# Performance work log

Hardware: AMD Instinct MI355X
Metric: run time of the kernel (lower is better)

The kernel has to match this reference:

```python
import jax, jax.numpy as jnp
import numpy as np

HIDDEN = 256
IN = 72  # 9*8
NUM_STEPS = 8


def setup_inputs() -> dict:
    key = jax.random.key(0)
    ks = jax.random.split(key, 12)
    s = 1.0 / np.sqrt(HIDDEN)
    B = 32768
    return {
        "z": jax.random.normal(ks[0], (1, B, HIDDEN), dtype=jnp.float32),
        # LSTM (torch layout): gates order i, f, g, o
        "W_ih": jax.random.uniform(ks[1], (4 * HIDDEN, IN), minval=-s, maxval=s),
        "W_hh": jax.random.uniform(ks[2], (4 * HIDDEN, HIDDEN), minval=-s, maxval=s),
        "b_ih": jax.random.uniform(ks[3], (4 * HIDDEN,), minval=-s, maxval=s),
        "b_hh": jax.random.uniform(ks[4], (4 * HIDDEN,), minval=-s, maxval=s),
        # Linear h: 256 -> 256
        "Wh": jax.random.uniform(ks[5], (HIDDEN, HIDDEN), minval=-s, maxval=s),
        "bh": jax.random.uniform(ks[6], (HIDDEN,), minval=-s, maxval=s),
        # Linear c: 256 -> 256
        "Wc": jax.random.uniform(ks[7], (HIDDEN, HIDDEN), minval=-s, maxval=s),
        "bc": jax.random.uniform(ks[8], (HIDDEN,), minval=-s, maxval=s),
        # Linear hout: 256 -> 72
        "Wo": jax.random.uniform(ks[9], (IN, HIDDEN), minval=-s, maxval=s),
        "bo": jax.random.uniform(ks[10], (IN,), minval=-s, maxval=s),
    }


def reference(z, W_ih, W_hh, b_ih, b_hh, Wh, bh, Wc, bc, Wo, bo):
    B = z.shape[1]
    z0 = z[0]                           # (B, 256)
    h = z0 @ Wh.T + bh                  # initial hidden state
    c = z0 @ Wc.T + bc                  # initial cell state
    x = jnp.zeros((B, IN), dtype=z.dtype)

    def step(carry, _):
        x, h, c = carry
        gates = x @ W_ih.T + b_ih + h @ W_hh.T + b_hh   # (B, 1024)
        i, f, g, o = jnp.split(gates, 4, axis=-1)
        i = jax.nn.sigmoid(i)
        f = jax.nn.sigmoid(f)
        g = jnp.tanh(g)
        o = jax.nn.sigmoid(o)
        c = f * c + i * g
        h = o * jnp.tanh(c)
        y = jax.nn.sigmoid(h @ Wo.T + bo)               # (B, 72), fed back as next input
        return (y, h, c), y

    _, ys = jax.lax.scan(step, (x, h, c), None, length=NUM_STEPS)  # (8, B, 72)
    return jnp.transpose(ys, (1, 0, 2))                             # (B, 8, 72)
```

## Files before the change

### kernel.cpp

```cpp
#include <hip/hip_runtime.h>
#include <hip/hip_bf16.h>

#define HID   256
#define NGATE 1024
#define INP   72
#define INPP  96
#define STEPS 8
#define TB    64
#define LDH   264
#define LDX   104

#define OFF_WHH 0
#define OFF_WIH 262144
#define OFF_WH  360448
#define OFF_WC  425984
#define OFF_WO  491520
#define N_BF    512000
#define OFF_BG_BYTES 1024000
#define OFF_STAGE_BYTES (1u << 20)

typedef short  s8_t  __attribute__((ext_vector_type(8)));
typedef float  f4_t  __attribute__((ext_vector_type(4)));

static __device__ __forceinline__ unsigned short f2bf(float f) {
  unsigned int u = __float_as_uint(f);
  u = (u + 0x7FFFu + ((u >> 16) & 1u)) >> 16;
  return (unsigned short)u;
}
static __device__ __forceinline__ float fast_rcp(float x) {
#if __has_builtin(__builtin_amdgcn_rcpf)
  return __builtin_amdgcn_rcpf(x);
#else
  return 1.f / x;
#endif
}
static __device__ __forceinline__ float sigm(float x) {
  return fast_rcp(1.f + __expf(-x));
}
static __device__ __forceinline__ float tanh_(float x) {
  float t = fminf(-2.f * x, 88.f);
  float e = __expf(t);
  return (1.f - e) * fast_rcp(1.f + e);
}

__global__ void prep_kernel(const float* __restrict__ Wih, const float* __restrict__ Whh,
                            const float* __restrict__ bih, const float* __restrict__ bhh,
                            const float* __restrict__ Wh, const float* __restrict__ Wc,
                            const float* __restrict__ Wo,
                            unsigned short* __restrict__ wsh, float* __restrict__ bg) {
  int stride = gridDim.x * blockDim.x;
  for (int i = blockIdx.x * blockDim.x + threadIdx.x; i < N_BF + NGATE; i += stride) {
    if (i < OFF_WIH) {
      wsh[i] = f2bf(Whh[i]);
    } else if (i < OFF_WH) {
      int j = i - OFF_WIH; int n = j / INPP; int k = j - n * INPP;
      wsh[i] = (k < INP) ? f2bf(Wih[n * INP + k]) : (unsigned short)0;
    } else if (i < OFF_WC) {
      wsh[i] = f2bf(Wh[i - OFF_WH]);
    } else if (i < OFF_WO) {
      wsh[i] = f2bf(Wc[i - OFF_WC]);
    } else if (i < N_BF) {
      int j = i - OFF_WO; int t = j >> 8; int k = j & 255;
      wsh[i] = (t < INP) ? f2bf(Wo[t * HID + k]) : (unsigned short)0;
    } else {
      int j = i - N_BF;
      bg[j] = bih[j] + bhh[j];
    }
  }
}

template <int STAGED>
__global__ __launch_bounds__(512, 2) void lstm_kernel(
    const float* __restrict__ z, const unsigned short* __restrict__ wsh,
    const float* __restrict__ bg, const float* __restrict__ bh,
    const float* __restrict__ bc, const float* __restrict__ bo,
    float* __restrict__ out, float* __restrict__ stage, int NB) {
  __shared__ unsigned short h_lds[TB * LDH];
  __shared__ unsigned short x_lds[TB * LDX];

  const int tid  = threadIdx.x;
  const int w    = tid >> 6;
  const int lane = tid & 63;
  const int lq   = lane >> 4;
  const int ln   = lane & 15;
  const int rb   = blockIdx.x * TB;
  const int colh0 = w * 32 + ln;

  const unsigned short* whh_l = wsh + OFF_WHH + colh0 * HID  + lq * 8;
  const unsigned short* wih_l = wsh + OFF_WIH + colh0 * INPP + lq * 8;
  const unsigned short* wh_l  = wsh + OFF_WH  + colh0 * HID  + lq * 8;
  const unsigned short* wc_l  = wsh + OFF_WC  + colh0 * HID  + lq * 8;
  const unsigned short* h_rd  = &h_lds[ln * LDH + lq * 8];
  const unsigned short* x_rd  = &x_lds[ln * LDX + lq * 8];
  unsigned short*       h_wr  = &h_lds[(lq * 4) * LDH + colh0];

  for (int i = tid; i < TB * LDX; i += 512) x_lds[i] = 0;

  f4_t acc_h[4][2], acc_c[4][2];
  #pragma unroll
  for (int rt = 0; rt < 4; ++rt)
    #pragma unroll
    for (int ct = 0; ct < 2; ++ct) {
      acc_h[rt][ct] = {0.f, 0.f, 0.f, 0.f};
      acc_c[rt][ct] = {0.f, 0.f, 0.f, 0.f};
    }

  const float* z_l = z + (size_t)(rb + ln) * HID + lq * 8;

  #pragma unroll 2
  for (int kc = 0; kc < 8; ++kc) {
    s8_t a[4];
    #pragma unroll
    for (int rt = 0; rt < 4; ++rt) {
      f4_t v0 = *reinterpret_cast<const f4_t*>(z_l + rt * 16 * HID + kc * 32);
      f4_t v1 = *reinterpret_cast<const f4_t*>(z_l + rt * 16 * HID + kc * 32 + 4);
      s8_t av;
      av[0] = (short)f2bf(v0[0]); av[1] = (short)f2bf(v0[1]);
      av[2] = (short)f2bf(v0[2]); av[3] = (short)f2bf(v0[3]);
      av[4] = (short)f2bf(v1[0]); av[5] = (short)f2bf(v1[1]);
      av[6] = (short)f2bf(v1[2]); av[7] = (short)f2bf(v1[3]);
      a[rt] = av;
    }
    #pragma unroll
    for (int ct = 0; ct < 2; ++ct) {
      s8_t bhf = *reinterpret_cast<const s8_t*>(wh_l + ct * 16 * HID + kc * 32);
      s8_t bcf = *reinterpret_cast<const s8_t*>(wc_l + ct * 16 * HID + kc * 32);
      #pragma unroll
      for (int rt = 0; rt < 4; ++rt) {
        acc_h[rt][ct] = __builtin_amdgcn_mfma_f32_16x16x32_bf16(a[rt], bhf, acc_h[rt][ct], 0, 0, 0);
        acc_c[rt][ct] = __builtin_amdgcn_mfma_f32_16x16x32_bf16(a[rt], bcf, acc_c[rt][ct], 0, 0, 0);
      }
    }
  }

  float c_reg[4][2][4];
  #pragma unroll
  for (int ct = 0; ct < 2; ++ct) {
    const float bhv = bh[colh0 + ct * 16];
    const float bcv = bc[colh0 + ct * 16];
    #pragma unroll
    for (int rt = 0; rt < 4; ++rt)
      #pragma unroll
      for (int r = 0; r < 4; ++r) {
        float hv = acc_h[rt][ct][r] + bhv;
        c_reg[rt][ct][r] = acc_c[rt][ct][r] + bcv;
        h_wr[(rt * 16 + r) * LDH + ct * 16] = f2bf(hv);
      }
  }
  __syncthreads();

  float biasg[4][2];
  #pragma unroll
  for (int q = 0; q < 4; ++q)
    #pragma unroll
    for (int ct = 0; ct < 2; ++ct)
      biasg[q][ct] = bg[q * 256 + colh0 + ct * 16];

  const int colY = w * 16 + ln;
  float bov = 0.f;
  const unsigned short* wo_l = wsh + OFF_WO + lq * 8;
  if (w < 5) {
    wo_l += colY * HID;
    if (colY < INP) bov = bo[colY];
  }

  for (int s = 0; s < STEPS; ++s) {
    f4_t acc[4][4][2];
    #pragma unroll
    for (int q = 0; q < 4; ++q)
      #pragma unroll
      for (int rt = 0; rt < 4; ++rt)
        #pragma unroll
        for (int ct = 0; ct < 2; ++ct) {
          const float b = biasg[q][ct];
          acc[q][rt][ct] = {b, b, b, b};
        }

    #pragma unroll 2
    for (int kc = 0; kc < 8; ++kc) {
      s8_t a[4];
      #pragma unroll
      for (int rt = 0; rt < 4; ++rt)
        a[rt] = *reinterpret_cast<const s8_t*>(h_rd + rt * 16 * LDH + kc * 32);
      #pragma unroll
      for (int q = 0; q < 4; ++q)
        #pragma unroll
        for (int ct = 0; ct < 2; ++ct) {
          s8_t bfr = *reinterpret_cast<const s8_t*>(whh_l + (q * 256 + ct * 16) * HID + kc * 32);
          #pragma unroll
          for (int rt = 0; rt < 4; ++rt)
            acc[q][rt][ct] = __builtin_amdgcn_mfma_f32_16x16x32_bf16(a[rt], bfr, acc[q][rt][ct], 0, 0, 0);
        }
    }
    #pragma unroll
    for (int kc = 0; kc < 3; ++kc) {
      s8_t a[4];
      #pragma unroll
      for (int rt = 0; rt < 4; ++rt)
        a[rt] = *reinterpret_cast<const s8_t*>(x_rd + rt * 16 * LDX + kc * 32);
      #pragma unroll
      for (int q = 0; q < 4; ++q)
        #pragma unroll
        for (int ct = 0; ct < 2; ++ct) {
          s8_t bfr = *reinterpret_cast<const s8_t*>(wih_l + (q * 256 + ct * 16) * INPP + kc * 32);
          #pragma unroll
          for (int rt = 0; rt < 4; ++rt)
            acc[q][rt][ct] = __builtin_amdgcn_mfma_f32_16x16x32_bf16(a[rt], bfr, acc[q][rt][ct], 0, 0, 0);
        }
    }
    __syncthreads();

    #pragma unroll
    for (int rt = 0; rt < 4; ++rt)
      #pragma unroll
      for (int ct = 0; ct < 2; ++ct)
        #pragma unroll
        for (int r = 0; r < 4; ++r) {
          float iv = sigm(acc[0][rt][ct][r]);
          float fv = sigm(acc[1][rt][ct][r]);
          float gv = tanh_(acc[2][rt][ct][r]);
          float ov = sigm(acc[3][rt][ct][r]);
          float cn = fv * c_reg[rt][ct][r] + iv * gv;
          c_reg[rt][ct][r] = cn;
          float hv = ov * tanh_(cn);
          h_wr[(rt * 16 + r) * LDH + ct * 16] = f2bf(hv);
        }
    __syncthreads();

    if (w < 5) {
      f4_t accy[4];
      #pragma unroll
      for (int rt = 0; rt < 4; ++rt) accy[rt] = {bov, bov, bov, bov};
      #pragma unroll 2
      for (int kc = 0; kc < 8; ++kc) {
        s8_t bfr = *reinterpret_cast<const s8_t*>(wo_l + kc * 32);
        #pragma unroll
        for (int rt = 0; rt < 4; ++rt) {
          s8_t a = *reinterpret_cast<const s8_t*>(h_rd + rt * 16 * LDH + kc * 32);
          accy[rt] = __builtin_amdgcn_mfma_f32_16x16x32_bf16(a, bfr, accy[rt], 0, 0, 0);
        }
      }
      if (colY < INP) {
        float* st_base;
        if (STAGED) {
          st_base = stage + (((size_t)s * NB + blockIdx.x) * TB + lq * 4) * INP + colY;
        } else {
          st_base = out + (size_t)(rb + lq * 4) * (STEPS * INP) + s * INP + colY;
        }
        unsigned short* x_wr = &x_lds[(lq * 4) * LDX + colY];
        #pragma unroll
        for (int rt = 0; rt < 4; ++rt)
          #pragma unroll
          for (int r = 0; r < 4; ++r) {
            float yv = sigm(accy[rt][r]);
            if (STAGED) {
              st_base[(size_t)(rt * 16 + r) * INP] = yv;
            } else {
              st_base[(size_t)(rt * 16 + r) * (STEPS * INP)] = yv;
            }
            x_wr[(rt * 16 + r) * LDX] = f2bf(yv);
          }
      }
    }
    __syncthreads();
  }
}

__global__ __launch_bounds__(512) void reorder_kernel(
    const float* __restrict__ stage, float* __restrict__ out, int NB) {
  const int lane = threadIdx.x & 63;
  const int row  = blockIdx.x * 8 + (threadIdx.x >> 6);
  const int b    = row >> 6;
  const int r    = row & 63;
  #pragma unroll
  for (int i = lane; i < STEPS * INP; i += 64) {
    int s = i / INP;
    int c = i - s * INP;
    out[(size_t)row * (STEPS * INP) + i] =
        stage[(((size_t)s * NB + b) * TB + r) * INP + c];
  }
}

extern "C" void kernel_launch(void* const* d_in, const int* in_sizes, int n_in,
                              void* d_out, int out_size, void* d_ws, size_t ws_size,
                              hipStream_t stream) {
  const float* z   = (const float*)d_in[0];
  const float* Wih = (const float*)d_in[1];
  const float* Whh = (const float*)d_in[2];
  const float* bih = (const float*)d_in[3];
  const float* bhh = (const float*)d_in[4];
  const float* Wh  = (const float*)d_in[5];
  const float* bh  = (const float*)d_in[6];
  const float* Wc  = (const float*)d_in[7];
  const float* bc  = (const float*)d_in[8];
  const float* Wo  = (const float*)d_in[9];
  const float* bo  = (const float*)d_in[10];
  float* out = (float*)d_out;

  unsigned short* wsh = (unsigned short*)d_ws;
  float* bg    = (float*)((char*)d_ws + OFF_BG_BYTES);
  float* stage = (float*)((char*)d_ws + OFF_STAGE_BYTES);

  const int B  = in_sizes[0] / HID;
  const int NB = B / TB;

  hipLaunchKernelGGL(prep_kernel, dim3(512), dim3(256), 0, stream,
                     Wih, Whh, bih, bhh, Wh, Wc, Wo, wsh, bg);

  const size_t stage_need = (size_t)OFF_STAGE_BYTES + (size_t)B * STEPS * INP * 4;
  if (ws_size >= stage_need) {
    hipLaunchKernelGGL((lstm_kernel<1>), dim3(NB), dim3(512), 0, stream,
                       z, wsh, bg, bh, bc, bo, out, stage, NB);
    hipLaunchKernelGGL(reorder_kernel, dim3(B / 8), dim3(512), 0, stream,
                       stage, out, NB);
  } else {
    hipLaunchKernelGGL((lstm_kernel<0>), dim3(NB), dim3(512), 0, stream,
                       z, wsh, bg, bh, bc, bo, out, stage, NB);
  }
}
```

Before: 680.7 us.

## Shrink LSTM row tile to 32 rows with 4 waves of 64 columns each

The batch tile per block drops from 64 to 32 rows and the block from 8 waves to 4, so each wave now owns 64 hidden columns over 2 row tiles instead of 32 columns over 4 row tiles. The output projection is remapped so all 4 waves compute 16 output columns each, and wave 0 computes the remaining 8. The aim is twice as many blocks, for better load balance across CUs and smaller LDS per block. In exchange each block streams the full recurrent weight matrix for half as many rows, doubling weight traffic per row, and wave 0 carries extra projection work that lengthens the serial step.

```diff
diff --git a/kernel.cpp b/kernel.cpp
--- a/kernel.cpp
+++ b/kernel.cpp
@@ -6,7 +6,8 @@
 #define INP   72
 #define INPP  96
 #define STEPS 8
-#define TB    64
+#define TB    32
+#define NTHR  256
 #define LDH   264
 #define LDX   104
 
@@ -70,7 +71,7 @@
 }
 
 template <int STAGED>
-__global__ __launch_bounds__(512, 2) void lstm_kernel(
+__global__ __launch_bounds__(NTHR, 2) void lstm_kernel(
     const float* __restrict__ z, const unsigned short* __restrict__ wsh,
     const float* __restrict__ bg, const float* __restrict__ bh,
     const float* __restrict__ bc, const float* __restrict__ bo,
@@ -84,7 +85,7 @@
   const int lq   = lane >> 4;
   const int ln   = lane & 15;
   const int rb   = blockIdx.x * TB;
-  const int colh0 = w * 32 + ln;
+  const int colh0 = w * 64 + ln;
 
   const unsigned short* whh_l = wsh + OFF_WHH + colh0 * HID  + lq * 8;
   const unsigned short* wih_l = wsh + OFF_WIH + colh0 * INPP + lq * 8;
@@ -94,13 +95,13 @@
   const unsigned short* x_rd  = &x_lds[ln * LDX + lq * 8];
   unsigned short*       h_wr  = &h_lds[(lq * 4) * LDH + colh0];
 
-  for (int i = tid; i < TB * LDX; i += 512) x_lds[i] = 0;
-
-  f4_t acc_h[4][2], acc_c[4][2];
+  for (int i = tid; i < TB * LDX; i += NTHR) x_lds[i] = 0;
+
+  f4_t acc_h[2][4], acc_c[2][4];
   #pragma unroll
-  for (int rt = 0; rt < 4; ++rt)
-    #pragma unroll
-    for (int ct = 0; ct < 2; ++ct) {
+  for (int rt = 0; rt < 2; ++rt)
+    #pragma unroll
+    for (int ct = 0; ct < 4; ++ct) {
       acc_h[rt][ct] = {0.f, 0.f, 0.f, 0.f};
       acc_c[rt][ct] = {0.f, 0.f, 0.f, 0.f};
     }
@@ -109,9 +110,9 @@
 
   #pragma unroll 2
   for (int kc = 0; kc < 8; ++kc) {
-    s8_t a[4];
-    #pragma unroll
-    for (int rt = 0; rt < 4; ++rt) {
+    s8_t a[2];
+    #pragma unroll
+    for (int rt = 0; rt < 2; ++rt) {
       f4_t v0 = *reinterpret_cast<const f4_t*>(z_l + rt * 16 * HID + kc * 32);
       f4_t v1 = *reinterpret_cast<const f4_t*>(z_l + rt * 16 * HID + kc * 32 + 4);
       s8_t av;
@@ -122,24 +123,24 @@
       a[rt] = av;
     }
     #pragma unroll
-    for (int ct = 0; ct < 2; ++ct) {
+    for (int ct = 0; ct < 4; ++ct) {
       s8_t bhf = *reinterpret_cast<const s8_t*>(wh_l + ct * 16 * HID + kc * 32);
       s8_t bcf = *reinterpret_cast<const s8_t*>(wc_l + ct * 16 * HID + kc * 32);
       #pragma unroll
-      for (int rt = 0; rt < 4; ++rt) {
+      for (int rt = 0; rt < 2; ++rt) {
         acc_h[rt][ct] = __builtin_amdgcn_mfma_f32_16x16x32_bf16(a[rt], bhf, acc_h[rt][ct], 0, 0, 0);
         acc_c[rt][ct] = __builtin_amdgcn_mfma_f32_16x16x32_bf16(a[rt], bcf, acc_c[rt][ct], 0, 0, 0);
       }
     }
   }
 
-  float c_reg[4][2][4];
+  float c_reg[2][4][4];
   #pragma unroll
-  for (int ct = 0; ct < 2; ++ct) {
+  for (int ct = 0; ct < 4; ++ct) {
     const float bhv = bh[colh0 + ct * 16];
     const float bcv = bc[colh0 + ct * 16];
     #pragma unroll
-    for (int rt = 0; rt < 4; ++rt)
+    for (int rt = 0; rt < 2; ++rt)
       #pragma unroll
       for (int r = 0; r < 4; ++r) {
         float hv = acc_h[rt][ct][r] + bhv;
@@ -149,71 +150,70 @@
   }
   __syncthreads();
 
-  float biasg[4][2];
+  float biasg[4][4];
   #pragma unroll
   for (int q = 0; q < 4; ++q)
     #pragma unroll
-    for (int ct = 0; ct < 2; ++ct)
+    for (int ct = 0; ct < 4; ++ct)
       biasg[q][ct] = bg[q * 256 + colh0 + ct * 16];
 
   const int colY = w * 16 + ln;
-  float bov = 0.f;
-  const unsigned short* wo_l = wsh + OFF_WO + lq * 8;
-  if (w < 5) {
-    wo_l += colY * HID;
-    if (colY < INP) bov = bo[colY];
-  }
+  const float bov = bo[colY];
+  const unsigned short* wo_l  = wsh + OFF_WO + colY * HID + lq * 8;
+  const int colY2 = 64 + ln;
+  const float bov2 = (colY2 < INP) ? bo[colY2] : 0.f;
+  const unsigned short* wo2_l = wsh + OFF_WO + colY2 * HID + lq * 8;
 
   for (int s = 0; s < STEPS; ++s) {
-    f4_t acc[4][4][2];
+    f4_t acc[4][2][4];
     #pragma unroll
     for (int q = 0; q < 4; ++q)
       #pragma unroll
-      for (int rt = 0; rt < 4; ++rt)
-        #pragma unroll
-        for (int ct = 0; ct < 2; ++ct) {
+      for (int rt = 0; rt < 2; ++rt)
+        #pragma unroll
+        for (int ct = 0; ct < 4; ++ct) {
           const float b = biasg[q][ct];
           acc[q][rt][ct] = {b, b, b, b};
         }
 
     #pragma unroll 2
     for (int kc = 0; kc < 8; ++kc) {
-      s8_t a[4];
-      #pragma unroll
-      for (int rt = 0; rt < 4; ++rt)
+      s8_t a[2];
+      #pragma unroll
+      for (int rt = 0; rt < 2; ++rt)
         a[rt] = *reinterpret_cast<const s8_t*>(h_rd + rt * 16 * LDH + kc * 32);
       #pragma unroll
       for (int q = 0; q < 4; ++q)
         #pragma unroll
-        for (int ct = 0; ct < 2; ++ct) {
+        for (int ct = 0; ct < 4; ++ct) {
           s8_t bfr = *reinterpret_cast<const s8_t*>(whh_l + (q * 256 + ct * 16) * HID + kc * 32);
           #pragma unroll
-          for (int rt = 0; rt < 4; ++rt)
+          for (int rt = 0; rt < 2; ++rt)
             acc[q][rt][ct] = __builtin_amdgcn_mfma_f32_16x16x32_bf16(a[rt], bfr, acc[q][rt][ct], 0, 0, 0);
         }
     }
     #pragma unroll
     for (int kc = 0; kc < 3; ++kc) {
-      s8_t a[4];
-      #pragma unroll
-      for (int rt = 0; rt < 4; ++rt)
+      s8_t a[2];
+      #pragma unroll
+      for (int rt = 0; rt < 2; ++rt)
         a[rt] = *reinterpret_cast<const s8_t*>(x_rd + rt * 16 * LDX + kc * 32);
       #pragma unroll
       for (int q = 0; q < 4; ++q)
         #pragma unroll
-        for (int ct = 0; ct < 2; ++ct) {
+        for (int ct = 0; ct < 4; ++ct) {
           s8_t bfr = *reinterpret_cast<const s8_t*>(wih_l + (q * 256 + ct * 16) * INPP + kc * 32);
           #pragma unroll
-          for (int rt = 0; rt < 4; ++rt)
+          for (int rt = 0; rt < 2; ++rt)
             acc[q][rt][ct] = __builtin_amdgcn_mfma_f32_16x16x32_bf16(a[rt], bfr, acc[q][rt][ct], 0, 0, 0);
         }
     }
     __syncthreads();
 
     #pragma unroll
-    for (int rt = 0; rt < 4; ++rt)
-      #pragma unroll
-      for (int ct = 0; ct < 2; ++ct)
+    for (int rt = 0; rt < 2; ++rt)
+      #pragma unroll
+      for (int ct = 0; ct < 4; ++ct)
         #pragma unroll
         for (int r = 0; r < 4; ++r) {
           float iv = sigm(acc[0][rt][ct][r]);
@@ -227,29 +227,62 @@
         }
     __syncthreads();
 
-    if (w < 5) {
-      f4_t accy[4];
-      #pragma unroll
-      for (int rt = 0; rt < 4; ++rt) accy[rt] = {bov, bov, bov, bov};
+    {
+      f4_t accy[2];
+      #pragma unroll
+      for (int rt = 0; rt < 2; ++rt) accy[rt] = {bov, bov, bov, bov};
       #pragma unroll 2
       for (int kc = 0; kc < 8; ++kc) {
         s8_t bfr = *reinterpret_cast<const s8_t*>(wo_l + kc * 32);
         #pragma unroll
-        for (int rt = 0; rt < 4; ++rt) {
+        for (int rt = 0; rt < 2; ++rt) {
           s8_t a = *reinterpret_cast<const s8_t*>(h_rd + rt * 16 * LDH + kc * 32);
           accy[rt] = __builtin_amdgcn_mfma_f32_16x16x32_bf16(a, bfr, accy[rt], 0, 0, 0);
         }
       }
-      if (colY < INP) {
+      float* st_base;
+      if (STAGED) {
+        st_base = stage + (((size_t)s * NB + blockIdx.x) * TB + lq * 4) * INP + colY;
+      } else {
+        st_base = out + (size_t)(rb + lq * 4) * (STEPS * INP) + s * INP + colY;
+      }
+      unsigned short* x_wr = &x_lds[(lq * 4) * LDX + colY];
+      #pragma unroll
+      for (int rt = 0; rt < 2; ++rt)
+        #pragma unroll
+        for (int r = 0; r < 4; ++r) {
+          float yv = sigm(accy[rt][r]);
+          if (STAGED) {
+            st_base[(size_t)(rt * 16 + r) * INP] = yv;
+          } else {
+            st_base[(size_t)(rt * 16 + r) * (STEPS * INP)] = yv;
+          }
+          x_wr[(rt * 16 + r) * LDX] = f2bf(yv);
+        }
+    }
+    if (w == 0) {
+      f4_t accy[2];
+      #pragma unroll
+      for (int rt = 0; rt < 2; ++rt) accy[rt] = {bov2, bov2, bov2, bov2};
+      #pragma unroll 2
+      for (int kc = 0; kc < 8; ++kc) {
+        s8_t bfr = *reinterpret_cast<const s8_t*>(wo2_l + kc * 32);
+        #pragma unroll
+        for (int rt = 0; rt < 2; ++rt) {
+          s8_t a = *reinterpret_cast<const s8_t*>(h_rd + rt * 16 * LDH + kc * 32);
+          accy[rt] = __builtin_amdgcn_mfma_f32_16x16x32_bf16(a, bfr, accy[rt], 0, 0, 0);
+        }
+      }
+      if (colY2 < INP) {
         float* st_base;
         if (STAGED) {
-          st_base = stage + (((size_t)s * NB + blockIdx.x) * TB + lq * 4) * INP + colY;
+          st_base = stage + (((size_t)s * NB + blockIdx.x) * TB + lq * 4) * INP + colY2;
         } else {
-          st_base = out + (size_t)(rb + lq * 4) * (STEPS * INP) + s * INP + colY;
-        }
-        unsigned short* x_wr = &x_lds[(lq * 4) * LDX + colY];
-        #pragma unroll
-        for (int rt = 0; rt < 4; ++rt)
+          st_base = out + (size_t)(rb + lq * 4) * (STEPS * INP) + s * INP + colY2;
+        }
+        unsigned short* x_wr = &x_lds[(lq * 4) * LDX + colY2];
+        #pragma unroll
+        for (int rt = 0; rt < 2; ++rt)
           #pragma unroll
           for (int r = 0; r < 4; ++r) {
             float yv = sigm(accy[rt][r]);
@@ -270,8 +303,8 @@
     const float* __restrict__ stage, float* __restrict__ out, int NB) {
   const int lane = threadIdx.x & 63;
   const int row  = blockIdx.x * 8 + (threadIdx.x >> 6);
-  const int b    = row >> 6;
-  const int r    = row & 63;
+  const int b    = row >> 5;
+  const int r    = row & 31;
   #pragma unroll
   for (int i = lane; i < STEPS * INP; i += 64) {
     int s = i / INP;
@@ -309,12 +342,12 @@
 
   const size_t stage_need = (size_t)OFF_STAGE_BYTES + (size_t)B * STEPS * INP * 4;
   if (ws_size >= stage_need) {
-    hipLaunchKernelGGL((lstm_kernel<1>), dim3(NB), dim3(512), 0, stream,
+    hipLaunchKernelGGL((lstm_kernel<1>), dim3(NB), dim3(NTHR), 0, stream,
                        z, wsh, bg, bh, bc, bo, out, stage, NB);
     hipLaunchKernelGGL(reorder_kernel, dim3(B / 8), dim3(512), 0, stream,
                        stage, out, NB);
   } else {
-    hipLaunchKernelGGL((lstm_kernel<0>), dim3(NB), dim3(512), 0, stream,
+    hipLaunchKernelGGL((lstm_kernel<0>), dim3(NB), dim3(NTHR), 0, stream,
                        z, wsh, bg, bh, bc, bo, out, stage, NB);
   }
 }
```

After: 1.092 ms. +60.4%, slower.

## Double block to 1024 threads and pre-swizzle weights into per-lane MFMA fragment order

Applied to the files above, without the earlier changes.

The block grows from 8 to 16 waves, and each wave now owns 16 hidden columns instead of 32. This halves the per-thread accumulator count, which lowers register pressure and allows more waves per CU (launch bounds 1024,4). The prep kernel rewrites all bf16 weights into a per-wave, per-lane fragment order so each B-fragment load is one fully contiguous 16-byte-per-lane read. The cost is more waves contending at each __syncthreads, and all 16 waves still stream the full weight set from L2 every step.

```diff
diff --git a/kernel.cpp b/kernel.cpp
--- a/kernel.cpp
+++ b/kernel.cpp
@@ -4,20 +4,18 @@
 #define HID   256
 #define NGATE 1024
 #define INP   72
-#define INPP  96
 #define STEPS 8
 #define TB    64
+#define NTHR  1024
 #define LDH   264
 #define LDX   104
 
-#define OFF_WHH 0
-#define OFF_WIH 262144
-#define OFF_WH  360448
-#define OFF_WC  425984
-#define OFF_WO  491520
-#define N_BF    512000
-#define OFF_BG_BYTES 1024000
-#define OFF_STAGE_BYTES (1u << 20)
+#define WSEQ2 32768
+#define OFF_WHI 524288
+#define OFF_WCI 589824
+#define N_ALL   655360
+#define OFF_BG_BYTES    1310720
+#define OFF_STAGE_BYTES 1314816
 
 typedef short  s8_t  __attribute__((ext_vector_type(8)));
 typedef float  f4_t  __attribute__((ext_vector_type(4)));
@@ -49,28 +47,58 @@
                             const float* __restrict__ Wo,
                             unsigned short* __restrict__ wsh, float* __restrict__ bg) {
   int stride = gridDim.x * blockDim.x;
-  for (int i = blockIdx.x * blockDim.x + threadIdx.x; i < N_BF + NGATE; i += stride) {
-    if (i < OFF_WIH) {
-      wsh[i] = f2bf(Whh[i]);
-    } else if (i < OFF_WH) {
-      int j = i - OFF_WIH; int n = j / INPP; int k = j - n * INPP;
-      wsh[i] = (k < INP) ? f2bf(Wih[n * INP + k]) : (unsigned short)0;
-    } else if (i < OFF_WC) {
-      wsh[i] = f2bf(Wh[i - OFF_WH]);
-    } else if (i < OFF_WO) {
-      wsh[i] = f2bf(Wc[i - OFF_WC]);
-    } else if (i < N_BF) {
-      int j = i - OFF_WO; int t = j >> 8; int k = j & 255;
-      wsh[i] = (t < INP) ? f2bf(Wo[t * HID + k]) : (unsigned short)0;
+  for (int i = blockIdx.x * blockDim.x + threadIdx.x; i < N_ALL + NGATE; i += stride) {
+    if (i < N_ALL) {
+      float v = 0.f;
+      if (i < OFF_WHI) {
+        int w  = i >> 15;
+        int r  = i & 32767;
+        int f  = r >> 9;
+        int e  = r & 511;
+        int lane = e >> 3, j = e & 7;
+        int lq = lane >> 4, ln = lane & 15;
+        int kk = lq * 8 + j;
+        if (f < 32) {
+          int kc = f >> 2, q = f & 3;
+          int g  = q * 256 + w * 16 + ln;
+          int k  = kc * 32 + kk;
+          v = Whh[g * HID + k];
+        } else if (f < 44) {
+          int t  = f - 32;
+          int kc = t >> 2, q = t & 3;
+          int g  = q * 256 + w * 16 + ln;
+          int k  = kc * 32 + kk;
+          v = (k < INP) ? Wih[g * INP + k] : 0.f;
+        } else if (f < 52) {
+          int kc = f - 44;
+          int c  = w * 16 + ln;
+          int k  = kc * 32 + kk;
+          v = (w < 5 && c < INP) ? Wo[c * HID + k] : 0.f;
+        }
+      } else {
+        int base = (i < OFF_WCI) ? OFF_WHI : OFF_WCI;
+        const float* Wsrc = (i < OFF_WCI) ? Wh : Wc;
+        int jj = i - base;
+        int w  = jj >> 12;
+        int r  = jj & 4095;
+        int kc = r >> 9;
+        int e  = r & 511;
+        int lane = e >> 3, j = e & 7;
+        int lq = lane >> 4, ln = lane & 15;
+        int c  = w * 16 + ln;
+        int k  = kc * 32 + lq * 8 + j;
+        v = Wsrc[c * HID + k];
+      }
+      wsh[i] = f2bf(v);
     } else {
-      int j = i - N_BF;
-      bg[j] = bih[j] + bhh[j];
+      int jb = i - N_ALL;
+      bg[jb] = bih[jb] + bhh[jb];
     }
   }
 }
 
 template <int STAGED>
-__global__ __launch_bounds__(512, 2) void lstm_kernel(
+__global__ __launch_bounds__(NTHR, 4) void lstm_kernel(
     const float* __restrict__ z, const unsigned short* __restrict__ wsh,
     const float* __restrict__ bg, const float* __restrict__ bh,
     const float* __restrict__ bc, const float* __restrict__ bo,
@@ -84,26 +112,23 @@
   const int lq   = lane >> 4;
   const int ln   = lane & 15;
   const int rb   = blockIdx.x * TB;
-  const int colh0 = w * 32 + ln;
-
-  const unsigned short* whh_l = wsh + OFF_WHH + colh0 * HID  + lq * 8;
-  const unsigned short* wih_l = wsh + OFF_WIH + colh0 * INPP + lq * 8;
-  const unsigned short* wh_l  = wsh + OFF_WH  + colh0 * HID  + lq * 8;
-  const unsigned short* wc_l  = wsh + OFF_WC  + colh0 * HID  + lq * 8;
-  const unsigned short* h_rd  = &h_lds[ln * LDH + lq * 8];
-  const unsigned short* x_rd  = &x_lds[ln * LDX + lq * 8];
-  unsigned short*       h_wr  = &h_lds[(lq * 4) * LDH + colh0];
-
-  for (int i = tid; i < TB * LDX; i += 512) x_lds[i] = 0;
-
-  f4_t acc_h[4][2], acc_c[4][2];
+  const int colh0 = w * 16 + ln;
+
+  const unsigned short* wst = wsh + w * WSEQ2 + lane * 8;
+  const unsigned short* whi = wsh + OFF_WHI + w * 4096 + lane * 8;
+  const unsigned short* wci = wsh + OFF_WCI + w * 4096 + lane * 8;
+  const unsigned short* h_rd = &h_lds[ln * LDH + lq * 8];
+  const unsigned short* x_rd = &x_lds[ln * LDX + lq * 8];
+  unsigned short*       h_wr = &h_lds[(lq * 4) * LDH + colh0];
+
+  for (int i = tid; i < TB * LDX; i += NTHR) x_lds[i] = 0;
+
+  f4_t acc_h[4], acc_c[4];
   #pragma unroll
-  for (int rt = 0; rt < 4; ++rt)
-    #pragma unroll
-    for (int ct = 0; ct < 2; ++ct) {
-      acc_h[rt][ct] = {0.f, 0.f, 0.f, 0.f};
-      acc_c[rt][ct] = {0.f, 0.f, 0.f, 0.f};
-    }
+  for (int rt = 0; rt < 4; ++rt) {
+    acc_h[rt] = {0.f, 0.f, 0.f, 0.f};
+    acc_c[rt] = {0.f, 0.f, 0.f, 0.f};
+  }
 
   const float* z_l = z + (size_t)(rb + ln) * HID + lq * 8;
 
@@ -121,60 +146,47 @@
       av[6] = (short)f2bf(v1[2]); av[7] = (short)f2bf(v1[3]);
       a[rt] = av;
     }
-    #pragma unroll
-    for (int ct = 0; ct < 2; ++ct) {
-      s8_t bhf = *reinterpret_cast<const s8_t*>(wh_l + ct * 16 * HID + kc * 32);
-      s8_t bcf = *reinterpret_cast<const s8_t*>(wc_l + ct * 16 * HID + kc * 32);
-      #pragma unroll
-      for (int rt = 0; rt < 4; ++rt) {
-        acc_h[rt][ct] = __builtin_amdgcn_mfma_f32_16x16x32_bf16(a[rt], bhf, acc_h[rt][ct], 0, 0, 0);
-        acc_c[rt][ct] = __builtin_amdgcn_mfma_f32_16x16x32_bf16(a[rt], bcf, acc_c[rt][ct], 0, 0, 0);
-      }
-    }
-  }
-
-  float c_reg[4][2][4];
-  #pragma unroll
-  for (int ct = 0; ct < 2; ++ct) {
-    const float bhv = bh[colh0 + ct * 16];
-    const float bcv = bc[colh0 + ct * 16];
+    s8_t bhf = *reinterpret_cast<const s8_t*>(whi + kc * 512);
+    s8_t bcf = *reinterpret_cast<const s8_t*>(wci + kc * 512);
+    #pragma unroll
+    for (int rt = 0; rt < 4; ++rt) {
+      acc_h[rt] = __builtin_amdgcn_mfma_f32_16x16x32_bf16(a[rt], bhf, acc_h[rt], 0, 0, 0);
+      acc_c[rt] = __builtin_amdgcn_mfma_f32_16x16x32_bf16(a[rt], bcf, acc_c[rt], 0, 0, 0);
+    }
+  }
+
+  float c_reg[4][4];
+  {
+    const float bhv = bh[colh0];
+    const float bcv = bc[colh0];
     #pragma unroll
     for (int rt = 0; rt < 4; ++rt)
       #pragma unroll
       for (int r = 0; r < 4; ++r) {
-        float hv = acc_h[rt][ct][r] + bhv;
-        c_reg[rt][ct][r] = acc_c[rt][ct][r] + bcv;
-        h_wr[(rt * 16 + r) * LDH + ct * 16] = f2bf(hv);
+        float hv = acc_h[rt][r] + bhv;
+        c_reg[rt][r] = acc_c[rt][r] + bcv;
+        h_wr[(rt * 16 + r) * LDH] = f2bf(hv);
       }
   }
   __syncthreads();
 
-  float biasg[4][2];
+  float biasg[4];
   #pragma unroll
   for (int q = 0; q < 4; ++q)
-    #pragma unroll
-    for (int ct = 0; ct < 2; ++ct)
-      biasg[q][ct] = bg[q * 256 + colh0 + ct * 16];
-
-  const int colY = w * 16 + ln;
+    biasg[q] = bg[q * 256 + colh0];
+
   float bov = 0.f;
-  const unsigned short* wo_l = wsh + OFF_WO + lq * 8;
-  if (w < 5) {
-    wo_l += colY * HID;
-    if (colY < INP) bov = bo[colY];
-  }
+  if (w < 5 && colh0 < INP) bov = bo[colh0];
 
   for (int s = 0; s < STEPS; ++s) {
-    f4_t acc[4][4][2];
+    f4_t acc[4][4];
     #pragma unroll
     for (int q = 0; q < 4; ++q)
       #pragma unroll
-      for (int rt = 0; rt < 4; ++rt)
-        #pragma unroll
-        for (int ct = 0; ct < 2; ++ct) {
-          const float b = biasg[q][ct];
-          acc[q][rt][ct] = {b, b, b, b};
-        }
+      for (int rt = 0; rt < 4; ++rt) {
+        const float b = biasg[q];
+        acc[q][rt] = {b, b, b, b};
+      }
 
     #pragma unroll 2
     for (int kc = 0; kc < 8; ++kc) {
@@ -183,14 +195,12 @@
       for (int rt = 0; rt < 4; ++rt)
         a[rt] = *reinterpret_cast<const s8_t*>(h_rd + rt * 16 * LDH + kc * 32);
       #pragma unroll
-      for (int q = 0; q < 4; ++q)
+      for (int q = 0; q < 4; ++q) {
+        s8_t bfr = *reinterpret_cast<const s8_t*>(wst + (kc * 4 + q) * 512);
         #pragma unroll
-        for (int ct = 0; ct < 2; ++ct) {
-          s8_t bfr = *reinterpret_cast<const s8_t*>(whh_l + (q * 256 + ct * 16) * HID + kc * 32);
-          #pragma unroll
-          for (int rt = 0; rt < 4; ++rt)
-            acc[q][rt][ct] = __builtin_amdgcn_mfma_f32_16x16x32_bf16(a[rt], bfr, acc[q][rt][ct], 0, 0, 0);
-        }
+        for (int rt = 0; rt < 4; ++rt)
+          acc[q][rt] = __builtin_amdgcn_mfma_f32_16x16x32_bf16(a[rt], bfr, acc[q][rt], 0, 0, 0);
+      }
     }
     #pragma unroll
     for (int kc = 0; kc < 3; ++kc) {
@@ -199,32 +209,28 @@
       for (int rt = 0; rt < 4; ++rt)
         a[rt] = *reinterpret_cast<const s8_t*>(x_rd + rt * 16 * LDX + kc * 32);
       #pragma unroll
-      for (int q = 0; q < 4; ++q)
+      for (int q = 0; q < 4; ++q) {
+        s8_t bfr = *reinterpret_cast<const s8_t*>(wst + (32 + kc * 4 + q) * 512);
         #pragma unroll
-        for (int ct = 0; ct < 2; ++ct) {
-          s8_t bfr = *reinterpret_cast<const s8_t*>(wih_l + (q * 256 + ct * 16) * INPP + kc * 32);
-          #pragma unroll
-          for (int rt = 0; rt < 4; ++rt)
-            acc[q][rt][ct] = __builtin_amdgcn_mfma_f32_16x16x32_bf16(a[rt], bfr, acc[q][rt][ct], 0, 0, 0);
-        }
+        for (int rt = 0; rt < 4; ++rt)
+          acc[q][rt] = __builtin_amdgcn_mfma_f32_16x16x32_bf16(a[rt], bfr, acc[q][rt], 0, 0, 0);
+      }
     }
     __syncthreads();
 
     #pragma unroll
     for (int rt = 0; rt < 4; ++rt)
       #pragma unroll
-      for (int ct = 0; ct < 2; ++ct)
-        #pragma unroll
-        for (int r = 0; r < 4; ++r) {
-          float iv = sigm(acc[0][rt][ct][r]);
-          float fv = sigm(acc[1][rt][ct][r]);
-          float gv = tanh_(acc[2][rt][ct][r]);
-          float ov = sigm(acc[3][rt][ct][r]);
-          float cn = fv * c_reg[rt][ct][r] + iv * gv;
-          c_reg[rt][ct][r] = cn;
-          float hv = ov * tanh_(cn);
-          h_wr[(rt * 16 + r) * LDH + ct * 16] = f2bf(hv);
-        }
+      for (int r = 0; r < 4; ++r) {
+        float iv = sigm(acc[0][rt][r]);
+        float fv = sigm(acc[1][rt][r]);
+        float gv = tanh_(acc[2][rt][r]);
+        float ov = sigm(acc[3][rt][r]);
+        float cn = fv * c_reg[rt][r] + iv * gv;
+        c_reg[rt][r] = cn;
+        float hv = ov * tanh_(cn);
+        h_wr[(rt * 16 + r) * LDH] = f2bf(hv);
+      }
     __syncthreads();
 
     if (w < 5) {
@@ -233,21 +239,21 @@
       for (int rt = 0; rt < 4; ++rt) accy[rt] = {bov, bov, bov, bov};
       #pragma unroll 2
       for (int kc = 0; kc < 8; ++kc) {
-        s8_t bfr = *reinterpret_cast<const s8_t*>(wo_l + kc * 32);
+        s8_t bfr = *reinterpret_cast<const s8_t*>(wst + (44 + kc) * 512);
         #pragma unroll
         for (int rt = 0; rt < 4; ++rt) {
           s8_t a = *reinterpret_cast<const s8_t*>(h_rd + rt * 16 * LDH + kc * 32);
           accy[rt] = __builtin_amdgcn_mfma_f32_16x16x32_bf16(a, bfr, accy[rt], 0, 0, 0);
         }
       }
-      if (colY < INP) {
+      if (colh0 < INP) {
         float* st_base;
         if (STAGED) {
-          st_base = stage + (((size_t)s * NB + blockIdx.x) * TB + lq * 4) * INP + colY;
+          st_base = stage + (((size_t)s * NB + blockIdx.x) * TB + lq * 4) * INP + colh0;
         } else {
-          st_base = out + (size_t)(rb + lq * 4) * (STEPS * INP) + s * INP + colY;
+          st_base = out + (size_t)(rb + lq * 4) * (STEPS * INP) + s * INP + colh0;
         }
-        unsigned short* x_wr = &x_lds[(lq * 4) * LDX + colY];
+        unsigned short* x_wr = &x_lds[(lq * 4) * LDX + colh0];
         #pragma unroll
         for (int rt = 0; rt < 4; ++rt)
           #pragma unroll
@@ -309,12 +315,12 @@
 
   const size_t stage_need = (size_t)OFF_STAGE_BYTES + (size_t)B * STEPS * INP * 4;
   if (ws_size >= stage_need) {
-    hipLaunchKernelGGL((lstm_kernel<1>), dim3(NB), dim3(512), 0, stream,
+    hipLaunchKernelGGL((lstm_kernel<1>), dim3(NB), dim3(NTHR), 0, stream,
                        z, wsh, bg, bh, bc, bo, out, stage, NB);
     hipLaunchKernelGGL(reorder_kernel, dim3(B / 8), dim3(512), 0, stream,
                        stage, out, NB);
   } else {
-    hipLaunchKernelGGL((lstm_kernel<0>), dim3(NB), dim3(512), 0, stream,
+    hipLaunchKernelGGL((lstm_kernel<0>), dim3(NB), dim3(NTHR), 0, stream,
                        z, wsh, bg, bh, bc, bo, out, stage, NB);
   }
 }
```

Measured after the change: 557.0 us. -18.2%, faster.
